# Optimization experiments

Measured on AMD Instinct MI355X. Metric: run time of the kernel, lower is better.

The kernel has to match this reference:

```python
import jax, jax.numpy as jnp
import numpy as np

C = 2048
N = 8
K = C // N  # 256
B = 4096


def setup_inputs() -> dict:
    key = jax.random.key(0)
    ks = jax.random.split(key, 9)
    s_in = 1.0 / np.sqrt(C)
    s_k = 1.0 / np.sqrt(K)
    return {
        "x": jax.random.normal(ks[0], (B, C), dtype=jnp.float32),
        # weights stored [in, out] (y = x @ W + b), equivalent to torch Linear
        "W_theta": jax.random.uniform(ks[1], (C, K), jnp.float32, -s_in, s_in),
        "b_theta": jax.random.uniform(ks[2], (K,), jnp.float32, -s_in, s_in),
        "W_phi": jax.random.uniform(ks[3], (C, K), jnp.float32, -s_in, s_in),
        "b_phi": jax.random.uniform(ks[4], (K,), jnp.float32, -s_in, s_in),
        "W_f": jax.random.uniform(ks[5], (C, K), jnp.float32, -s_in, s_in),
        "b_f": jax.random.uniform(ks[6], (K,), jnp.float32, -s_in, s_in),
        "W_g": jax.random.uniform(ks[7], (K, C), jnp.float32, -s_k, s_k),
        "b_g": jax.random.uniform(ks[8], (C,), jnp.float32, -s_k, s_k),
    }


def reference(x, W_theta, b_theta, W_phi, b_phi, W_f, b_f, W_g, b_g):
    theta = x @ W_theta + b_theta          # [B, K]
    phi = x @ W_phi + b_phi                # [B, K]
    f = x @ W_f + b_f                      # [B, K]
    # outer product per sample -> [B, K, K], softmax over last dim
    scores = jax.nn.softmax(theta[:, :, None] * phi[:, None, :], axis=-1)
    t = jnp.einsum('bij,bj->bi', scores, f)  # [B, K]
    return x + t @ W_g + b_g               # residual, [B, C]
```

## Files before the change

kernel.cpp:

```cpp
#include <hip/hip_runtime.h>

constexpr int Bsz   = 4096;
constexpr int Cdim  = 2048;
constexpr int Kdim  = 256;
constexpr int PROJW = 3 * Kdim;
constexpr int KSPLIT = 4;

typedef __attribute__((ext_vector_type(8))) short short8;
typedef __attribute__((ext_vector_type(4))) float floatx4;

__device__ __forceinline__ unsigned short f2bf(float f) {
    unsigned int u = __float_as_uint(f);
    u += 0x7FFFu + ((u >> 16) & 1u);
    return (unsigned short)(u >> 16);
}

__device__ __forceinline__ void load16(const void* g, void* lds) {
    __builtin_amdgcn_global_load_lds(
        (const __attribute__((address_space(1))) unsigned int*)g,
        (__attribute__((address_space(3))) unsigned int*)lds, 16, 0, 0);
}

__global__ __launch_bounds__(256) void prep_kernel(
    const float* __restrict__ x, unsigned short* __restrict__ xb,
    const float* __restrict__ Wt, const float* __restrict__ Wp,
    const float* __restrict__ Wf, const float* __restrict__ Wg,
    unsigned short* __restrict__ Wcat, unsigned short* __restrict__ WgT)
{
    __shared__ float tile[32][33];
    const int bid = blockIdx.x;
    if (bid < 8192) {
        const int i = bid * 256 + threadIdx.x;
        float4 v = reinterpret_cast<const float4*>(x)[i];
        ushort4 o;
        o.x = f2bf(v.x); o.y = f2bf(v.y); o.z = f2bf(v.z); o.w = f2bf(v.w);
        reinterpret_cast<ushort4*>(xb)[i] = o;
        return;
    }
    const int q = bid - 8192;
    const int z = q >> 9;
    const int tileId = q & 511;
    const float* __restrict__ in;
    unsigned short* __restrict__ out;
    int R, C;
    if (z < 3) {
        in = (z == 0) ? Wt : (z == 1) ? Wp : Wf;
        out = Wcat + (size_t)z * Kdim * Cdim;
        R = Cdim; C = Kdim;
    } else {
        in = Wg; out = WgT; R = Kdim; C = Cdim;
    }
    const int ctiles = C / 32;
    const int c0 = (tileId % ctiles) * 32;
    const int r0 = (tileId / ctiles) * 32;
    const int tx = threadIdx.x & 31, ty = threadIdx.x >> 5;
#pragma unroll
    for (int i = ty; i < 32; i += 8)
        tile[i][tx] = in[(size_t)(r0 + i) * C + c0 + tx];
    __syncthreads();
#pragma unroll
    for (int i = ty; i < 32; i += 8)
        out[(size_t)(c0 + i) * R + r0 + tx] = f2bf(tile[tx][i]);
}

__global__ __launch_bounds__(256) void proj_mfma(
    const unsigned short* __restrict__ xb,
    const unsigned short* __restrict__ Wcat,
    float* __restrict__ pp)
{
    __shared__ short As[128 * 32];
    __shared__ short Bs[128 * 32];

    const int tid  = threadIdx.x;
    const int lane = tid & 63;
    const int wid  = tid >> 6;
    const int wr   = wid >> 1, wc = wid & 1;
    const int rowBase = blockIdx.x * 128;
    const int colBase = blockIdx.y * 128;
    const int k0      = blockIdx.z * (Cdim / KSPLIT);

    floatx4 acc[4][4] = {};

    const unsigned short* gA0 = xb   + (size_t)(rowBase + (tid >> 2)) * Cdim + k0 + (tid & 3) * 8;
    const unsigned short* gA1 = xb   + (size_t)(rowBase + 64 + (tid >> 2)) * Cdim + k0 + (tid & 3) * 8;
    const unsigned short* gB0 = Wcat + (size_t)(colBase + (tid >> 2)) * Cdim + k0 + (tid & 3) * 8;
    const unsigned short* gB1 = Wcat + (size_t)(colBase + 64 + (tid >> 2)) * Cdim + k0 + (tid & 3) * 8;

    short* ldsA0 = As + ((tid & ~63)) * 8;
    short* ldsA1 = As + (256 + (tid & ~63)) * 8;
    short* ldsB0 = Bs + ((tid & ~63)) * 8;
    short* ldsB1 = Bs + (256 + (tid & ~63)) * 8;

    const int mrow = lane & 15;
    const int kgrp = lane >> 4;

    for (int kt = 0; kt < Cdim / KSPLIT; kt += 32) {
        load16(gA0, ldsA0); load16(gA1, ldsA1);
        load16(gB0, ldsB0); load16(gB1, ldsB1);
        gA0 += 32; gA1 += 32; gB0 += 32; gB1 += 32;
        __syncthreads();

        short8 af[4], bfr[4];
#pragma unroll
        for (int i = 0; i < 4; ++i)
            af[i]  = *(const short8*)&As[(wr * 64 + i * 16 + mrow) * 32 + kgrp * 8];
#pragma unroll
        for (int j = 0; j < 4; ++j)
            bfr[j] = *(const short8*)&Bs[(wc * 64 + j * 16 + mrow) * 32 + kgrp * 8];
#pragma unroll
        for (int i = 0; i < 4; ++i)
#pragma unroll
            for (int j = 0; j < 4; ++j)
                acc[i][j] = __builtin_amdgcn_mfma_f32_16x16x32_bf16(
                    af[i], bfr[j], acc[i][j], 0, 0, 0);
        __syncthreads();
    }

    float* __restrict__ dst = pp + (size_t)blockIdx.z * Bsz * PROJW;
#pragma unroll
    for (int j = 0; j < 4; ++j) {
        const int col = colBase + wc * 64 + j * 16 + mrow;
#pragma unroll
        for (int i = 0; i < 4; ++i) {
#pragma unroll
            for (int r = 0; r < 4; ++r) {
                const int row = rowBase + wr * 64 + i * 16 + kgrp * 4 + r;
                dst[(size_t)row * PROJW + col] = acc[i][j][r];
            }
        }
    }
}

__global__ __launch_bounds__(256) void attn_kernel(
    const float* __restrict__ pp,
    const float* __restrict__ bt, const float* __restrict__ bp,
    const float* __restrict__ bff,
    unsigned short* __restrict__ t)
{
    __shared__ float2 spf[4][Kdim];

    const int tid = threadIdx.x;
    const int s   = tid >> 6;
    const int l   = tid & 63;
    const int b   = blockIdx.x * 4 + s;
    const size_t rowOff = (size_t)b * PROJW;

    float tl[4];
#pragma unroll
    for (int i = 0; i < 4; ++i) {
        const int j = l + i * 64;
        float th = bt[j], ph = bp[j], fv = bff[j];
#pragma unroll
        for (int z = 0; z < KSPLIT; ++z) {
            const float* __restrict__ r = pp + (size_t)z * Bsz * PROJW + rowOff;
            th += r[j];
            ph += r[Kdim + j];
            fv += r[2 * Kdim + j];
        }
        tl[i] = th * 1.44269504f;
        spf[s][j] = make_float2(ph, fv);
    }
    __syncthreads();

    float2 sa[4] = {}, na[4] = {};
    const float2* __restrict__ sp = spf[s];
#pragma unroll 4
    for (int k = 0; k < Kdim; k += 2) {
        const float4 v = *reinterpret_cast<const float4*>(&sp[k]);
#pragma unroll
        for (int i = 0; i < 4; ++i) {
            const float e0 = __builtin_amdgcn_exp2f(tl[i] * v.x);
            const float e1 = __builtin_amdgcn_exp2f(tl[i] * v.z);
            sa[i].x += e0;
            sa[i].y += e1;
            na[i].x = fmaf(e0, v.y, na[i].x);
            na[i].y = fmaf(e1, v.w, na[i].y);
        }
    }
#pragma unroll
    for (int i = 0; i < 4; ++i) {
        const int j = l + i * 64;
        t[(size_t)b * Kdim + j] = f2bf((na[i].x + na[i].y) / (sa[i].x + sa[i].y));
    }
}

__global__ __launch_bounds__(256) void out_mfma(
    const unsigned short* __restrict__ tb,
    const unsigned short* __restrict__ WgT,
    const float* __restrict__ bg,
    const float* __restrict__ x,
    float* __restrict__ out)
{
    __shared__ short As[128 * 32];
    __shared__ short Bs[128 * 32];

    const int tid  = threadIdx.x;
    const int lane = tid & 63;
    const int wid  = tid >> 6;
    const int wr   = wid >> 1, wc = wid & 1;
    const int rowBase = blockIdx.x * 128;
    const int colBase = blockIdx.y * 128;

    floatx4 acc[4][4] = {};

    const unsigned short* gA0 = tb  + (size_t)(rowBase + (tid >> 2)) * Kdim + (tid & 3) * 8;
    const unsigned short* gA1 = tb  + (size_t)(rowBase + 64 + (tid >> 2)) * Kdim + (tid & 3) * 8;
    const unsigned short* gB0 = WgT + (size_t)(colBase + (tid >> 2)) * Kdim + (tid & 3) * 8;
    const unsigned short* gB1 = WgT + (size_t)(colBase + 64 + (tid >> 2)) * Kdim + (tid & 3) * 8;

    short* ldsA0 = As + ((tid & ~63)) * 8;
    short* ldsA1 = As + (256 + (tid & ~63)) * 8;
    short* ldsB0 = Bs + ((tid & ~63)) * 8;
    short* ldsB1 = Bs + (256 + (tid & ~63)) * 8;

    const int mrow = lane & 15;
    const int kgrp = lane >> 4;

    for (int kt = 0; kt < Kdim; kt += 32) {
        load16(gA0, ldsA0); load16(gA1, ldsA1);
        load16(gB0, ldsB0); load16(gB1, ldsB1);
        gA0 += 32; gA1 += 32; gB0 += 32; gB1 += 32;
        __syncthreads();

        short8 af[4], bfr[4];
#pragma unroll
        for (int i = 0; i < 4; ++i)
            af[i]  = *(const short8*)&As[(wr * 64 + i * 16 + mrow) * 32 + kgrp * 8];
#pragma unroll
        for (int j = 0; j < 4; ++j)
            bfr[j] = *(const short8*)&Bs[(wc * 64 + j * 16 + mrow) * 32 + kgrp * 8];
#pragma unroll
        for (int i = 0; i < 4; ++i)
#pragma unroll
            for (int j = 0; j < 4; ++j)
                acc[i][j] = __builtin_amdgcn_mfma_f32_16x16x32_bf16(
                    af[i], bfr[j], acc[i][j], 0, 0, 0);
        __syncthreads();
    }

#pragma unroll
    for (int j = 0; j < 4; ++j) {
        const int col = colBase + wc * 64 + j * 16 + mrow;
        const float bv = bg[col];
#pragma unroll
        for (int i = 0; i < 4; ++i) {
#pragma unroll
            for (int r = 0; r < 4; ++r) {
                const int row = rowBase + wr * 64 + i * 16 + kgrp * 4 + r;
                out[(size_t)row * Cdim + col] =
                    acc[i][j][r] + bv + x[(size_t)row * Cdim + col];
            }
        }
    }
}

extern "C" void kernel_launch(void* const* d_in, const int* in_sizes, int n_in,
                              void* d_out, int out_size, void* d_ws, size_t ws_size,
                              hipStream_t stream) {
    const float* x  = (const float*)d_in[0];
    const float* Wt = (const float*)d_in[1];
    const float* bt = (const float*)d_in[2];
    const float* Wp = (const float*)d_in[3];
    const float* bp = (const float*)d_in[4];
    const float* Wf = (const float*)d_in[5];
    const float* bf = (const float*)d_in[6];
    const float* Wg = (const float*)d_in[7];
    const float* bg = (const float*)d_in[8];
    float* out = (float*)d_out;

    char* w = (char*)d_ws;
    float*          pp   = (float*)w;
    unsigned short* xb   = (unsigned short*)(w + 50331648);
    unsigned short* Wcat = (unsigned short*)(w + 67108864);
    unsigned short* WgT  = (unsigned short*)(w + 70254592);
    unsigned short* tb   = (unsigned short*)(w + 71303168);

    prep_kernel<<<10240, 256, 0, stream>>>(x, xb, Wt, Wp, Wf, Wg, Wcat, WgT);
    proj_mfma<<<dim3(Bsz / 128, PROJW / 128, KSPLIT), 256, 0, stream>>>(xb, Wcat, pp);
    attn_kernel<<<Bsz / 4, 256, 0, stream>>>(pp, bt, bp, bf, tb);
    out_mfma<<<dim3(Bsz / 128, Cdim / 128), 256, 0, stream>>>(tb, WgT, bg, x, out);
}
```

Measured before the change: 179.9 us.

## Store split-K projection partials in fp16 and vectorize attention kernel loads/math

```diff
diff --git a/kernel.cpp b/kernel.cpp
--- a/kernel.cpp
+++ b/kernel.cpp
@@ -8,6 +8,8 @@
 
 typedef __attribute__((ext_vector_type(8))) short short8;
 typedef __attribute__((ext_vector_type(4))) float floatx4;
+typedef __attribute__((ext_vector_type(2))) float float2v;
+typedef __attribute__((ext_vector_type(4))) _Float16 half4v;
 
 __device__ __forceinline__ unsigned short f2bf(float f) {
     unsigned int u = __float_as_uint(f);
@@ -66,7 +68,7 @@
 __global__ __launch_bounds__(256) void proj_mfma(
     const unsigned short* __restrict__ xb,
     const unsigned short* __restrict__ Wcat,
-    float* __restrict__ pp)
+    _Float16* __restrict__ pp)
 {
     __shared__ short As[128 * 32];
     __shared__ short Bs[128 * 32];
@@ -116,7 +118,7 @@
         __syncthreads();
     }
 
-    float* __restrict__ dst = pp + (size_t)blockIdx.z * Bsz * PROJW;
+    _Float16* __restrict__ dst = pp + (size_t)blockIdx.z * Bsz * PROJW;
 #pragma unroll
     for (int j = 0; j < 4; ++j) {
         const int col = colBase + wc * 64 + j * 16 + mrow;
@@ -125,63 +127,69 @@
 #pragma unroll
             for (int r = 0; r < 4; ++r) {
                 const int row = rowBase + wr * 64 + i * 16 + kgrp * 4 + r;
-                dst[(size_t)row * PROJW + col] = acc[i][j][r];
+                dst[(size_t)row * PROJW + col] = (_Float16)acc[i][j][r];
             }
         }
     }
 }
 
 __global__ __launch_bounds__(256) void attn_kernel(
-    const float* __restrict__ pp,
+    const _Float16* __restrict__ pp,
     const float* __restrict__ bt, const float* __restrict__ bp,
     const float* __restrict__ bff,
     unsigned short* __restrict__ t)
 {
-    __shared__ float2 spf[4][Kdim];
+    __shared__ float4 spf[4][Kdim / 2];
 
     const int tid = threadIdx.x;
     const int s   = tid >> 6;
     const int l   = tid & 63;
     const int b   = blockIdx.x * 4 + s;
+    const int j0  = l * 4;
     const size_t rowOff = (size_t)b * PROJW;
 
-    float tl[4];
-#pragma unroll
-    for (int i = 0; i < 4; ++i) {
-        const int j = l + i * 64;
-        float th = bt[j], ph = bp[j], fv = bff[j];
-#pragma unroll
-        for (int z = 0; z < KSPLIT; ++z) {
-            const float* __restrict__ r = pp + (size_t)z * Bsz * PROJW + rowOff;
-            th += r[j];
-            ph += r[Kdim + j];
-            fv += r[2 * Kdim + j];
+    float4 th = *reinterpret_cast<const float4*>(bt + j0);
+    float4 ph = *reinterpret_cast<const float4*>(bp + j0);
+    float4 fv = *reinterpret_cast<const float4*>(bff + j0);
+#pragma unroll
+    for (int z = 0; z < KSPLIT; ++z) {
+        const _Float16* __restrict__ r = pp + (size_t)z * Bsz * PROJW + rowOff;
+        half4v a = *reinterpret_cast<const half4v*>(r + j0);
+        half4v c = *reinterpret_cast<const half4v*>(r + Kdim + j0);
+        half4v d = *reinterpret_cast<const half4v*>(r + 2 * Kdim + j0);
+        th.x += (float)a.x; th.y += (float)a.y; th.z += (float)a.z; th.w += (float)a.w;
+        ph.x += (float)c.x; ph.y += (float)c.y; ph.z += (float)c.z; ph.w += (float)c.w;
+        fv.x += (float)d.x; fv.y += (float)d.y; fv.z += (float)d.z; fv.w += (float)d.w;
+    }
+    const float tl[4] = {th.x * 1.44269504f, th.y * 1.44269504f,
+                         th.z * 1.44269504f, th.w * 1.44269504f};
+    spf[s][2 * l]     = make_float4(ph.x, fv.x, ph.y, fv.y);
+    spf[s][2 * l + 1] = make_float4(ph.z, fv.z, ph.w, fv.w);
+    __syncthreads();
+
+    float2v sa[4] = {}, na[4] = {};
+    const float4* __restrict__ sp = spf[s];
+#pragma unroll 4
+    for (int p = 0; p < Kdim / 2; ++p) {
+        const float4 v = sp[p];
+        const float2v ph2 = {v.x, v.z};
+        const float2v ff2 = {v.y, v.w};
+#pragma unroll
+        for (int i = 0; i < 4; ++i) {
+            const float2v a = tl[i] * ph2;
+            float2v e;
+            e.x = __builtin_amdgcn_exp2f(a.x);
+            e.y = __builtin_amdgcn_exp2f(a.y);
+            sa[i] += e;
+            na[i] += e * ff2;
         }
-        tl[i] = th * 1.44269504f;
-        spf[s][j] = make_float2(ph, fv);
-    }
-    __syncthreads();
-
-    float2 sa[4] = {}, na[4] = {};
-    const float2* __restrict__ sp = spf[s];
-#pragma unroll 4
-    for (int k = 0; k < Kdim; k += 2) {
-        const float4 v = *reinterpret_cast<const float4*>(&sp[k]);
-#pragma unroll
-        for (int i = 0; i < 4; ++i) {
-            const float e0 = __builtin_amdgcn_exp2f(tl[i] * v.x);
-            const float e1 = __builtin_amdgcn_exp2f(tl[i] * v.z);
-            sa[i].x += e0;
-            sa[i].y += e1;
-            na[i].x = fmaf(e0, v.y, na[i].x);
-            na[i].y = fmaf(e1, v.w, na[i].y);
-        }
-    }
-#pragma unroll
-    for (int i = 0; i < 4; ++i) {
-        const int j = l + i * 64;
-        t[(size_t)b * Kdim + j] = f2bf((na[i].x + na[i].y) / (sa[i].x + sa[i].y));
-    }
+    }
+    ushort4 o;
+    unsigned short* op = &o.x;
+#pragma unroll
+    for (int i = 0; i < 4; ++i)
+        op[i] = f2bf((na[i].x + na[i].y) / (sa[i].x + sa[i].y));
+    *reinterpret_cast<ushort4*>(t + (size_t)b * Kdim + j0) = o;
 }
 
 __global__ __launch_bounds__(256) void out_mfma(
@@ -269,11 +277,11 @@
     float* out = (float*)d_out;
 
     char* w = (char*)d_ws;
-    float*          pp   = (float*)w;
-    unsigned short* xb   = (unsigned short*)(w + 50331648);
-    unsigned short* Wcat = (unsigned short*)(w + 67108864);
-    unsigned short* WgT  = (unsigned short*)(w + 70254592);
-    unsigned short* tb   = (unsigned short*)(w + 71303168);
+    _Float16*       pp   = (_Float16*)w;
+    unsigned short* xb   = (unsigned short*)(w + 25165824);
+    unsigned short* Wcat = (unsigned short*)(w + 41943040);
+    unsigned short* WgT  = (unsigned short*)(w + 45088768);
+    unsigned short* tb   = (unsigned short*)(w + 46137344);
 
     prep_kernel<<<10240, 256, 0, stream>>>(x, xb, Wt, Wp, Wf, Wg, Wcat, WgT);
     proj_mfma<<<dim3(Bsz / 128, PROJW / 128, KSPLIT), 256, 0, stream>>>(xb, Wcat, pp);
```

New measurement: 168.6 us. 1.07x faster.
